# Performance work log

Hardware: AMD Instinct MI355X
Metric: run time of the kernel (lower is better)

Reference implementation:

```python
import jax, jax.numpy as jnp
import numpy as np
import math

# ---- architecture constants (match init_kwargs defaults of OfficialMamba3SISO) ----
D_MODEL = 1024
D_STATE = 128
EXPAND = 2
HEADDIM = 64
NGROUPS = 1
D_INNER = EXPAND * D_MODEL              # 2048
NHEADS = D_INNER // HEADDIM             # 32
ROPE_FRACTION = 0.5
SPLIT = int(D_STATE * ROPE_FRACTION)    # rotary span of the state dim
SPLIT -= SPLIT % 2                      # 64
NUM_ANGLES = SPLIT // 2                 # 32
A_FLOOR = 1e-4
EPS = 1e-5
DT_MIN, DT_MAX, DT_INIT_FLOOR = 1e-3, 1e-1, 1e-4
D_IN_PROJ = 2 * D_INNER + 2 * D_STATE * NGROUPS + 3 * NHEADS + NUM_ANGLES  # 4480


def _rmsnorm(x, w):
    xf = x.astype(jnp.float32)
    return xf * jax.lax.rsqrt(jnp.mean(xf * xf, axis=-1, keepdims=True) + EPS) * w


def _rope(v, theta):
    # rotate first SPLIT dims of the state axis by cumulative angles theta [..., NUM_ANGLES]
    v1 = v[..., :NUM_ANGLES]
    v2 = v[..., NUM_ANGLES:SPLIT]
    rest = v[..., SPLIT:]
    c, s = jnp.cos(theta), jnp.sin(theta)
    return jnp.concatenate([v1 * c - v2 * s, v1 * s + v2 * c, rest], axis=-1)


def setup_inputs() -> dict:
    key = jax.random.key(0)
    ks = jax.random.split(key, 6)
    b, l = 2, 1024
    u = jax.random.normal(ks[0], (b, l, D_MODEL), jnp.float32)
    W_in = jax.random.normal(ks[1], (D_IN_PROJ, D_MODEL), jnp.float32) * 0.02
    W_out = jax.random.normal(ks[2], (D_MODEL, D_INNER), jnp.float32) * 0.02
    # dt_bias init exactly as in the torch module
    _dt = jnp.exp(jax.random.uniform(ks[3], (NHEADS,), jnp.float32)
                  * (math.log(DT_MAX) - math.log(DT_MIN)) + math.log(DT_MIN))
    _dt = jnp.clip(_dt, DT_INIT_FLOOR, None)
    dt_bias = _dt + jnp.log(-jnp.expm1(-_dt))
    B_bias = jnp.ones((NHEADS, D_STATE), jnp.float32)   # mimo_rank=1 squeezed
    C_bias = jnp.ones((NHEADS, D_STATE), jnp.float32)
    B_norm_w = jnp.ones((D_STATE,), jnp.float32)
    C_norm_w = jnp.ones((D_STATE,), jnp.float32)
    D_param = jnp.ones((NHEADS,), jnp.float32)
    return {"u": u, "W_in": W_in, "W_out": W_out, "dt_bias": dt_bias,
            "B_bias": B_bias, "C_bias": C_bias, "B_norm_w": B_norm_w,
            "C_norm_w": C_norm_w, "D_param": D_param}


def reference(u, W_in, W_out, dt_bias, B_bias, C_bias, B_norm_w, C_norm_w, D_param):
    b, l, _ = u.shape
    proj = u @ W_in.T                                   # [b,l,4480]
    sizes = [D_INNER, D_INNER, D_STATE * NGROUPS, D_STATE * NGROUPS,
             NHEADS, NHEADS, NHEADS, NUM_ANGLES]
    splits = np.cumsum(sizes)[:-1]
    z, x, B, C, dd_dt, dd_A, trap, angles = jnp.split(proj, splits, axis=-1)
    z = z.reshape(b, l, NHEADS, HEADDIM)
    x = x.reshape(b, l, NHEADS, HEADDIM)
    B = B.reshape(b, l, NGROUPS, D_STATE)
    C = C.reshape(b, l, NGROUPS, D_STATE)

    a = -jax.nn.softplus(dd_A.astype(jnp.float32))
    a = jnp.minimum(a, -A_FLOOR)                        # [b,l,h]
    dt = jax.nn.softplus(dd_dt.astype(jnp.float32) + dt_bias)  # [b,l,h]
    adt = a * dt

    # RoPE-style angle cumsum: theta_t = sum_{s<=t} angle_s * dt_s (per head)
    theta = jnp.cumsum(angles[:, :, None, :].astype(jnp.float32) * dt[..., None], axis=1)  # [b,l,h,na]

    Bn = _rmsnorm(B, B_norm_w)                          # [b,l,g,n]
    Cn = _rmsnorm(C, C_norm_w)
    head_group = np.repeat(np.arange(NGROUPS), NHEADS // NGROUPS)
    Bh = Bn[:, :, head_group, :] + B_bias               # [b,l,h,n]
    Ch = Cn[:, :, head_group, :] + C_bias
    Bh = _rope(Bh, theta)
    Ch = _rope(Ch, theta)

    lam = jax.nn.sigmoid(trap.astype(jnp.float32))      # trapezoidal mixing, [b,l,h]
    g = jnp.exp(adt)                                    # decay, [b,l,h]

    xs = (jnp.moveaxis(x.astype(jnp.float32), 1, 0), jnp.moveaxis(Bh, 1, 0),
          jnp.moveaxis(Ch, 1, 0), jnp.moveaxis(dt, 1, 0),
          jnp.moveaxis(g, 1, 0), jnp.moveaxis(lam, 1, 0))
    h0 = jnp.zeros((b, NHEADS, HEADDIM, D_STATE), jnp.float32)
    bx0 = jnp.zeros_like(h0)

    def step(carry, inp):
        h, bx_prev = carry
        x_t, B_t, C_t, dt_t, g_t, lam_t = inp
        bx_t = x_t[..., :, None] * B_t[..., None, :]    # outer product [b,h,p,n]
        ge = g_t[..., None, None]
        dte = dt_t[..., None, None]
        le = lam_t[..., None, None]
        # generalized trapezoidal discretization (Mamba-3):
        # h_t = g_t h_{t-1} + dt_t * (lam_t B_t x_t + (1-lam_t) g_t B_{t-1} x_{t-1})
        h = ge * h + dte * (le * bx_t + (1.0 - le) * ge * bx_prev)
        y_t = jnp.einsum('bhpn,bhn->bhp', h, C_t)
        return (h, bx_t), y_t

    _, ys = jax.lax.scan(step, (h0, bx0), xs)
    y = jnp.moveaxis(ys, 0, 1) + D_param[:, None] * x   # skip term, [b,l,h,p]
    y = y * jax.nn.silu(z)                              # gated output (Z passed to kernel)
    y = y.reshape(b, l, D_INNER).astype(u.dtype)
    return y @ W_out.T
```

## Files before the change

kernel.cpp:

```cpp
#include <hip/hip_runtime.h>
#include <hip/hip_bf16.h>
#include <math.h>

#define BATCH 2
#define SEQ 1024
#define DMODEL 1024
#define DSTATE 128
#define HEADDIM 64
#define NHEADS 32
#define DINNER 2048
#define NUMANG 32
#define DPROJ 4480
#define CH 64
#define NCH 16
#define TAILSTART 4352
#define OFF_Z 0
#define OFF_X 2048
#define OFF_B 4096
#define OFF_C 4224
#define OFF_DT 4352
#define OFF_A 4384
#define OFF_TRAP 4416
#define OFF_ANG 4448

typedef __attribute__((ext_vector_type(8))) short bf16x8;
typedef __attribute__((ext_vector_type(4))) float f32x4;
typedef unsigned short u16;

__device__ __forceinline__ u16 f2bf(float f) {
  unsigned int u = __float_as_uint(f);
  u += 0x7FFFu + ((u >> 16) & 1u);
  return (u16)(u >> 16);
}
__device__ __forceinline__ float bf2f(u16 x) {
  return __uint_as_float(((unsigned int)x) << 16);
}

__global__ __launch_bounds__(256) void cvt_bf16(const float* __restrict__ in,
                                                u16* __restrict__ out, int n4) {
  int i = blockIdx.x * 256 + threadIdx.x;
  if (i >= n4) return;
  float4 v = ((const float4*)in)[i];
  ushort4 o;
  o.x = f2bf(v.x); o.y = f2bf(v.y); o.z = f2bf(v.z); o.w = f2bf(v.w);
  ((ushort4*)out)[i] = o;
}

__device__ __forceinline__ void gload_lds16(const void* g, void* l) {
  __builtin_amdgcn_global_load_lds(
      (const __attribute__((address_space(1))) unsigned int*)g,
      (__attribute__((address_space(3))) unsigned int*)l, 16, 0, 0);
}

__global__ __launch_bounds__(256) void gemm_proj64(const u16* __restrict__ A,
                                                   const u16* __restrict__ B,
                                                   u16* __restrict__ Cb,
                                                   float* __restrict__ tailF,
                                                   int M, int N, int K) {
  __shared__ u16 As[64 * 64];
  __shared__ u16 Bs[64 * 64];
  const int tid = threadIdx.x;
  const int lane = tid & 63, wave = tid >> 6;
  const int bm = blockIdx.y * 64, bn = blockIdx.x * 64;
  const int wm = (wave >> 1) * 32, wn = (wave & 1) * 32;
  const int srow = wave * 8 + (lane >> 3);
  const int scol = (((lane & 7) ^ ((lane >> 3) & 7)) * 8);
  const u16* Ab = A + (size_t)(bm + srow) * K + scol;
  const u16* Bb = B + (size_t)(bn + srow) * K + scol;
  u16* Asw = As + wave * 512;
  u16* Bsw = Bs + wave * 512;
  f32x4 acc[2][2];
#pragma unroll
  for (int i = 0; i < 2; ++i)
#pragma unroll
    for (int j = 0; j < 2; ++j) acc[i][j] = (f32x4){0.f, 0.f, 0.f, 0.f};
  const int fr = lane & 15, fq = lane >> 4, sw = fr & 7;

  for (int k0 = 0; k0 < K; k0 += 64) {
    __syncthreads();
#pragma unroll
    for (int it = 0; it < 2; ++it) {
      gload_lds16(Ab + (size_t)(it * 32) * K + k0, Asw + it * 2048);
      gload_lds16(Bb + (size_t)(it * 32) * K + k0, Bsw + it * 2048);
    }
    __syncthreads();
#pragma unroll
    for (int kh = 0; kh < 2; ++kh) {
      bf16x8 af[2], bfv[2];
#pragma unroll
      for (int i = 0; i < 2; ++i)
        af[i] = *(const bf16x8*)(As + (wm + i * 16 + fr) * 64 + (((kh * 4 + fq) ^ sw) * 8));
#pragma unroll
      for (int j = 0; j < 2; ++j)
        bfv[j] = *(const bf16x8*)(Bs + (wn + j * 16 + fr) * 64 + (((kh * 4 + fq) ^ sw) * 8));
#pragma unroll
      for (int i = 0; i < 2; ++i)
#pragma unroll
        for (int j = 0; j < 2; ++j)
          acc[i][j] = __builtin_amdgcn_mfma_f32_16x16x32_bf16(af[i], bfv[j], acc[i][j], 0, 0, 0);
    }
  }
  const int orow = bm + wm + fq * 4;
  const int ocol = bn + wn + fr;
  const bool tail = (bn >= TAILSTART);
#pragma unroll
  for (int i = 0; i < 2; ++i)
#pragma unroll
    for (int j = 0; j < 2; ++j)
#pragma unroll
      for (int r = 0; r < 4; ++r) {
        float v = acc[i][j][r];
        int row = orow + i * 16 + r, col = ocol + j * 16;
        Cb[(size_t)row * N + col] = f2bf(v);
        if (tail) tailF[(size_t)row * 128 + (col - TAILSTART)] = v;
      }
}

__global__ __launch_bounds__(256) void gemm_out64(const u16* __restrict__ A,
                                                  const u16* __restrict__ B,
                                                  float* __restrict__ C,
                                                  int M, int N, int K) {
  __shared__ u16 As[64 * 64];
  __shared__ u16 Bs[64 * 64];
  const int tid = threadIdx.x;
  const int lane = tid & 63, wave = tid >> 6;
  const int bm = blockIdx.y * 64, bn = blockIdx.x * 64;
  const int wm = (wave >> 1) * 32, wn = (wave & 1) * 32;
  const int srow = wave * 8 + (lane >> 3);
  const int scol = (((lane & 7) ^ ((lane >> 3) & 7)) * 8);
  const u16* Ab = A + (size_t)(bm + srow) * K + scol;
  const u16* Bb = B + (size_t)(bn + srow) * K + scol;
  u16* Asw = As + wave * 512;
  u16* Bsw = Bs + wave * 512;
  f32x4 acc[2][2];
#pragma unroll
  for (int i = 0; i < 2; ++i)
#pragma unroll
    for (int j = 0; j < 2; ++j) acc[i][j] = (f32x4){0.f, 0.f, 0.f, 0.f};
  const int fr = lane & 15, fq = lane >> 4, sw = fr & 7;

  for (int k0 = 0; k0 < K; k0 += 64) {
    __syncthreads();
#pragma unroll
    for (int it = 0; it < 2; ++it) {
      gload_lds16(Ab + (size_t)(it * 32) * K + k0, Asw + it * 2048);
      gload_lds16(Bb + (size_t)(it * 32) * K + k0, Bsw + it * 2048);
    }
    __syncthreads();
#pragma unroll
    for (int kh = 0; kh < 2; ++kh) {
      bf16x8 af[2], bfv[2];
#pragma unroll
      for (int i = 0; i < 2; ++i)
        af[i] = *(const bf16x8*)(As + (wm + i * 16 + fr) * 64 + (((kh * 4 + fq) ^ sw) * 8));
#pragma unroll
      for (int j = 0; j < 2; ++j)
        bfv[j] = *(const bf16x8*)(Bs + (wn + j * 16 + fr) * 64 + (((kh * 4 + fq) ^ sw) * 8));
#pragma unroll
      for (int i = 0; i < 2; ++i)
#pragma unroll
        for (int j = 0; j < 2; ++j)
          acc[i][j] = __builtin_amdgcn_mfma_f32_16x16x32_bf16(af[i], bfv[j], acc[i][j], 0, 0, 0);
    }
  }
  const int orow = bm + wm + fq * 4;
  const int ocol = bn + wn + fr;
#pragma unroll
  for (int i = 0; i < 2; ++i)
#pragma unroll
    for (int j = 0; j < 2; ++j)
#pragma unroll
      for (int r = 0; r < 4; ++r)
        C[(size_t)(orow + i * 16 + r) * N + ocol + j * 16] = acc[i][j][r];
}

__device__ __forceinline__ float softplusf(float x) {
  return fmaxf(x, 0.f) + log1pf(expf(-fabsf(x)));
}

__global__ __launch_bounds__(1024) void theta_kernel(const float* __restrict__ tailF,
                                                     const float* __restrict__ dt_bias,
                                                     float4* __restrict__ sc4,
                                                     float4* __restrict__ theta4) {
  __shared__ float4 part[16];
  __shared__ float4 part2[16];
  const int blk = blockIdx.x;
  const int bh = blk >> 3, kc = blk & 7;
  const int b = bh >> 5, h = bh & 31;
  const int l = threadIdx.x;
  const int lane = l & 63, w = l >> 6;
  const float* trow = tailF + (size_t)(b * SEQ + l) * 128;
  float ddt = trow[h];
  float dt = softplusf(ddt + dt_bias[h]);
  if (kc == 0) {
    float dda = trow[32 + h];
    float trp = trow[64 + h];
    float a = fminf(-softplusf(dda), -1e-4f);
    float adt = a * dt;
    float lam = 1.0f / (1.0f + expf(-trp));
    sc4[(size_t)bh * SEQ + l] = make_float4(dt, expf(adt), lam, adt);
  }
  float4 v = *(const float4*)(trow + 96 + kc * 4);
  v.x *= dt; v.y *= dt; v.z *= dt; v.w *= dt;
#pragma unroll
  for (int off = 1; off < 64; off <<= 1) {
    float tx = __shfl_up(v.x, off, 64);
    float ty = __shfl_up(v.y, off, 64);
    float tz = __shfl_up(v.z, off, 64);
    float tw = __shfl_up(v.w, off, 64);
    if (lane >= off) { v.x += tx; v.y += ty; v.z += tz; v.w += tw; }
  }
  if (lane == 63) part[w] = v;
  __syncthreads();
  if (l < 16) {
    float4 p = part[l];
#pragma unroll
    for (int off = 1; off < 16; off <<= 1) {
      float tx = __shfl_up(p.x, off, 16);
      float ty = __shfl_up(p.y, off, 16);
      float tz = __shfl_up(p.z, off, 16);
      float tw = __shfl_up(p.w, off, 16);
      if (l >= off) { p.x += tx; p.y += ty; p.z += tz; p.w += tw; }
    }
    part2[l] = p;
  }
  __syncthreads();
  if (w > 0) {
    float4 o = part2[w - 1];
    v.x += o.x; v.y += o.y; v.z += o.z; v.w += o.w;
  }
  theta4[((size_t)(b * SEQ + l) * NHEADS + h) * 8 + kc] = v;
}

__global__ __launch_bounds__(1024) void rope_kernel(const u16* __restrict__ proj16,
                                                    const float* __restrict__ theta,
                                                    const float* __restrict__ B_bias,
                                                    const float* __restrict__ C_bias,
                                                    const float* __restrict__ Bnw,
                                                    const float* __restrict__ Cnw,
                                                    u16* __restrict__ Bh,
                                                    u16* __restrict__ Ch) {
  const int bl = blockIdx.x;
  const int b = bl >> 10, l = bl & 1023;
  const int tid = threadIdx.x;
  __shared__ float sB[128], sC[128], red[4];
  __shared__ float cth[1024], sth[1024];
  float bv = 0.f, cv = 0.f;
  const size_t row = (size_t)bl * DPROJ;
  if (tid < 128) {
    bv = bf2f(proj16[row + OFF_B + tid]);
    cv = bf2f(proj16[row + OFF_C + tid]);
    float sb = bv * bv, sc = cv * cv;
    for (int m = 32; m; m >>= 1) { sb += __shfl_xor(sb, m); sc += __shfl_xor(sc, m); }
    const int wave = tid >> 6;
    if ((tid & 63) == 0) { red[wave * 2] = sb; red[wave * 2 + 1] = sc; }
  }
  {
    float th = theta[(size_t)bl * 1024 + tid];
    cth[tid] = cosf(th);
    sth[tid] = sinf(th);
  }
  __syncthreads();
  if (tid < 128) {
    float rb = rsqrtf((red[0] + red[2]) / 128.0f + 1e-5f);
    float rc = rsqrtf((red[1] + red[3]) / 128.0f + 1e-5f);
    sB[tid] = bv * rb * Bnw[tid];
    sC[tid] = cv * rc * Cnw[tid];
  }
  __syncthreads();
  const int h = tid >> 5;
  const int n0 = (tid & 31) * 4;
  float ob[4], oc[4];
  if (n0 < 32) {
#pragma unroll
    for (int j = 0; j < 4; ++j) {
      int n = n0 + j;
      float c = cth[h * 32 + n], s = sth[h * 32 + n];
      float b1 = sB[n] + B_bias[h * 128 + n];
      float b2 = sB[n + 32] + B_bias[h * 128 + n + 32];
      float c1 = sC[n] + C_bias[h * 128 + n];
      float c2 = sC[n + 32] + C_bias[h * 128 + n + 32];
      ob[j] = b1 * c - b2 * s;
      oc[j] = c1 * c - c2 * s;
    }
  } else if (n0 < 64) {
#pragma unroll
    for (int j = 0; j < 4; ++j) {
      int n = n0 + j, k = n - 32;
      float c = cth[h * 32 + k], s = sth[h * 32 + k];
      float b1 = sB[k] + B_bias[h * 128 + k];
      float b2 = sB[k + 32] + B_bias[h * 128 + k + 32];
      float c1 = sC[k] + C_bias[h * 128 + k];
      float c2 = sC[k + 32] + C_bias[h * 128 + k + 32];
      ob[j] = b1 * s + b2 * c;
      oc[j] = c1 * s + c2 * c;
    }
  } else {
#pragma unroll
    for (int j = 0; j < 4; ++j) {
      int n = n0 + j;
      ob[j] = sB[n] + B_bias[h * 128 + n];
      oc[j] = sC[n] + C_bias[h * 128 + n];
    }
  }
  size_t o = (((size_t)(b * NHEADS + h)) * SEQ + l) * DSTATE + n0;
  ushort4 vb = {f2bf(ob[0]), f2bf(ob[1]), f2bf(ob[2]), f2bf(ob[3])};
  ushort4 vc = {f2bf(oc[0]), f2bf(oc[1]), f2bf(oc[2]), f2bf(oc[3])};
  *(ushort4*)&Bh[o] = vb;
  *(ushort4*)&Ch[o] = vc;
}

#define SWB 136
#define SWS 72

__global__ __launch_bounds__(256) void chunk_kernel(
    const u16* __restrict__ proj16,
    const float4* __restrict__ sc4,
    const u16* __restrict__ Bh16,
    const u16* __restrict__ Ch16,
    u16* __restrict__ Ybuf,
    float* __restrict__ dHT,
    float* __restrict__ Gv_g,
    float2* __restrict__ de_g) {
  __shared__ u16 sCb[64 * SWB];
  __shared__ u16 sBb[64 * SWB];
  __shared__ u16 sBt[128 * SWS];
  __shared__ u16 sXt[64 * SWS];
  __shared__ u16 sSw[64 * SWS];
  __shared__ float sA[64], sW[64], sDL[64], sCV[64];

  const int blk = blockIdx.x;
  const int bh = blk >> 4, ch = blk & 15;
  const int b = bh >> 5, h = bh & 31;
  const int t0 = ch * CH;
  const int tid = threadIdx.x;
  const int lane = tid & 63, wave = tid >> 6;

  {
    const int row = tid >> 5;
    const int c4 = tid & 31;
#pragma unroll
    for (int pass = 0; pass < 8; ++pass) {
      int ll = pass * 8 + row;
      int l = t0 + ll;
      ushort4 cv = *(const ushort4*)&Ch16[((size_t)bh * SEQ + l) * DSTATE + c4 * 4];
      ushort4 bv = *(const ushort4*)&Bh16[((size_t)bh * SEQ + l) * DSTATE + c4 * 4];
      *(ushort4*)&sCb[ll * SWB + c4 * 4] = cv;
      *(ushort4*)&sBb[ll * SWB + c4 * 4] = bv;
      sBt[(c4 * 4 + 0) * SWS + ll] = bv.x;
      sBt[(c4 * 4 + 1) * SWS + ll] = bv.y;
      sBt[(c4 * 4 + 2) * SWS + ll] = bv.z;
      sBt[(c4 * 4 + 3) * SWS + ll] = bv.w;
    }
    const int xr = tid >> 2, xc = tid & 3;
    const u16* xrow = &proj16[(size_t)(b * SEQ + t0 + xr) * DPROJ + OFF_X + h * 64];
#pragma unroll
    for (int j = 0; j < 4; ++j) {
      ushort4 xv = *(const ushort4*)(xrow + xc * 16 + j * 4);
      int p = xc * 16 + j * 4;
      sXt[(p + 0) * SWS + xr] = xv.x;
      sXt[(p + 1) * SWS + xr] = xv.y;
      sXt[(p + 2) * SWS + xr] = xv.z;
      sXt[(p + 3) * SWS + xr] = xv.w;
    }
  }
  if (tid < 64) {
    float4 s = sc4[(size_t)bh * SEQ + t0 + tid];
    float dt = s.x, lam = s.z, adt = s.w;
    float A = adt;
#pragma unroll
    for (int off = 1; off < 64; off <<= 1) {
      float t = __shfl_up(A, off, 64);
      if (tid >= off) A += t;
    }
    float dtn = __shfl_down(dt, 1, 64);
    float lamn = __shfl_down(lam, 1, 64);
    float dl = dt * lam;
    float w = dl + dtn * (1.0f - lamn);
    if (tid == 63) w = 0.0f;
    float A63 = __shfl(A, 63, 64);
    float cv = (tid < 63) ? expf(A63 - A) * w : dl;
    sA[tid] = A; sW[tid] = w; sCV[tid] = cv; sDL[tid] = dl;
    Gv_g[((size_t)bh * NCH + ch) * 64 + tid] = expf(A);
    if (tid == 0) de_g[(size_t)bh * NCH + ch] = make_float2(expf(A63), dt * (1.0f - lam));
  }
  __syncthreads();

  const int fr = lane & 15, fq = lane >> 4;

  {
    f32x4 acc[4];
#pragma unroll
    for (int j = 0; j < 4; ++j) acc[j] = (f32x4){0.f, 0.f, 0.f, 0.f};
#pragma unroll
    for (int kc = 0; kc < 4; ++kc) {
      bf16x8 af = *(const bf16x8*)&sBb[(wave * 16 + fr) * SWB + kc * 32 + fq * 8];
#pragma unroll
      for (int j = 0; j < 4; ++j) {
        bf16x8 bf = *(const bf16x8*)&sCb[(j * 16 + fr) * SWB + kc * 32 + fq * 8];
        acc[j] = __builtin_amdgcn_mfma_f32_16x16x32_bf16(af, bf, acc[j], 0, 0, 0);
      }
    }
    const int sbase = wave * 16 + fq * 4;
#pragma unroll
    for (int j = 0; j < 4; ++j) {
      int t = j * 16 + fr;
      float At = sA[t], dlt = sDL[t];
#pragma unroll
      for (int r = 0; r < 4; ++r) {
        int ss = sbase + r;
        float f = (ss < t) ? expf(At - sA[ss]) * sW[ss] : ((ss == t) ? dlt : 0.0f);
        sSw[t * SWS + ss] = f2bf(acc[j][r] * f);
      }
    }
  }
  __syncthreads();

  {
    f32x4 acc[4];
#pragma unroll
    for (int j = 0; j < 4; ++j) acc[j] = (f32x4){0.f, 0.f, 0.f, 0.f};
#pragma unroll
    for (int kc = 0; kc < 2; ++kc) {
      bf16x8 af = *(const bf16x8*)&sSw[(wave * 16 + fr) * SWS + kc * 32 + fq * 8];
#pragma unroll
      for (int j = 0; j < 4; ++j) {
        bf16x8 bf = *(const bf16x8*)&sXt[(j * 16 + fr) * SWS + kc * 32 + fq * 8];
        acc[j] = __builtin_amdgcn_mfma_f32_16x16x32_bf16(af, bf, acc[j], 0, 0, 0);
      }
    }
    const int tr = t0 + wave * 16 + fq * 4;
#pragma unroll
    for (int j = 0; j < 4; ++j) {
      int p = j * 16 + fr;
#pragma unroll
      for (int r = 0; r < 4; ++r)
        Ybuf[(size_t)(b * SEQ + tr + r) * DINNER + h * 64 + p] = f2bf(acc[j][r]);
    }
  }
  __syncthreads();

  {
    const int p = tid >> 2;
    const int s0 = (tid & 3) * 16;
#pragma unroll
    for (int k = 0; k < 16; ++k) {
      int s = s0 + k;
      sXt[p * SWS + s] = f2bf(bf2f(sXt[p * SWS + s]) * sCV[s]);
    }
  }
  __syncthreads();

  {
#pragma unroll
    for (int mi = 0; mi < 2; ++mi) {
      f32x4 acc[4];
#pragma unroll
      for (int j = 0; j < 4; ++j) acc[j] = (f32x4){0.f, 0.f, 0.f, 0.f};
      const int nrow = wave * 32 + mi * 16;
#pragma unroll
      for (int kc = 0; kc < 2; ++kc) {
        bf16x8 af = *(const bf16x8*)&sBt[(nrow + fr) * SWS + kc * 32 + fq * 8];
#pragma unroll
        for (int j = 0; j < 4; ++j) {
          bf16x8 bf = *(const bf16x8*)&sXt[(j * 16 + fr) * SWS + kc * 32 + fq * 8];
          acc[j] = __builtin_amdgcn_mfma_f32_16x16x32_bf16(af, bf, acc[j], 0, 0, 0);
        }
      }
      const int nr = nrow + fq * 4;
#pragma unroll
      for (int j = 0; j < 4; ++j) {
        int p = j * 16 + fr;
#pragma unroll
        for (int r = 0; r < 4; ++r)
          dHT[(((size_t)bh * NCH + ch) * 128 + nr + r) * 64 + p] = acc[j][r];
      }
    }
  }
}

__global__ __launch_bounds__(512) void carry_kernel(
    const u16* __restrict__ proj16,
    const u16* __restrict__ Bh16,
    const float* __restrict__ dHT,
    const float2* __restrict__ de_g,
    float* __restrict__ Heff) {
  const int bh = blockIdx.x;
  const int b = bh >> 5, h = bh & 31;
  const int tid = threadIdx.x;
  const int n = tid >> 2;
  const int p0 = (tid & 3) * 16;
  float hreg[16] = {};
  for (int c = 0; c < NCH; ++c) {
    float2 de = de_g[bh * NCH + c];
    float heff[16];
    if (c == 0) {
#pragma unroll
      for (int j = 0; j < 16; ++j) heff[j] = 0.0f;
    } else {
      int lprev = c * CH - 1;
      float Bp = bf2f(Bh16[((size_t)bh * SEQ + lprev) * DSTATE + n]);
      const u16* xp = &proj16[(size_t)(b * SEQ + lprev) * DPROJ + OFF_X + h * 64 + p0];
      float eB = de.y * Bp;
#pragma unroll
      for (int j4 = 0; j4 < 4; ++j4) {
        ushort4 xv = *(const ushort4*)(xp + j4 * 4);
        heff[j4 * 4 + 0] = hreg[j4 * 4 + 0] + eB * bf2f(xv.x);
        heff[j4 * 4 + 1] = hreg[j4 * 4 + 1] + eB * bf2f(xv.y);
        heff[j4 * 4 + 2] = hreg[j4 * 4 + 2] + eB * bf2f(xv.z);
        heff[j4 * 4 + 3] = hreg[j4 * 4 + 3] + eB * bf2f(xv.w);
      }
    }
    size_t base = (((size_t)bh * NCH + c) * 128 + n) * 64 + p0;
#pragma unroll
    for (int j4 = 0; j4 < 4; ++j4)
      *(float4*)&Heff[base + j4 * 4] = *(const float4*)&heff[j4 * 4];
#pragma unroll
    for (int j4 = 0; j4 < 4; ++j4) {
      float4 dh = *(const float4*)&dHT[base + j4 * 4];
      hreg[j4 * 4 + 0] = de.x * heff[j4 * 4 + 0] + dh.x;
      hreg[j4 * 4 + 1] = de.x * heff[j4 * 4 + 1] + dh.y;
      hreg[j4 * 4 + 2] = de.x * heff[j4 * 4 + 2] + dh.z;
      hreg[j4 * 4 + 3] = de.x * heff[j4 * 4 + 3] + dh.w;
    }
  }
}

__global__ __launch_bounds__(256) void inter_kernel(
    const u16* __restrict__ proj16,
    const u16* __restrict__ Ch16,
    const float* __restrict__ Heff,
    const float* __restrict__ Gv_g,
    const float* __restrict__ Dp,
    u16* __restrict__ Ybuf) {
  __shared__ float sC[64][132];
  __shared__ float sH[128][68];
  __shared__ float sGv[64];
  const int blk = blockIdx.x;
  const int bh = blk >> 4, ch = blk & 15;
  const int b = bh >> 5, h = bh & 31;
  const int t0 = ch * CH;
  const int tid = threadIdx.x;
  {
    const int row = tid >> 5, c4 = tid & 31;
#pragma unroll
    for (int pass = 0; pass < 8; ++pass) {
      int l = t0 + pass * 8 + row;
      ushort4 cv = *(const ushort4*)&Ch16[((size_t)bh * SEQ + l) * DSTATE + c4 * 4];
      float4 cf = {bf2f(cv.x), bf2f(cv.y), bf2f(cv.z), bf2f(cv.w)};
      *(float4*)&sC[pass * 8 + row][c4 * 4] = cf;
    }
    const int hr = tid >> 4, hc = tid & 15;
#pragma unroll
    for (int pass = 0; pass < 8; ++pass) {
      int n = pass * 16 + hr;
      float4 hv = *(const float4*)&Heff[(((size_t)bh * NCH + ch) * 128 + n) * 64 + hc * 4];
      *(float4*)&sH[n][hc * 4] = hv;
    }
    if (tid < 64) sGv[tid] = Gv_g[((size_t)bh * NCH + ch) * 64 + tid];
  }
  __syncthreads();
  const int ty = tid >> 4, tx = tid & 15;
  float acc[4][4] = {};
  for (int n = 0; n < 128; n += 4) {
    float4 cv[4], hv[4];
#pragma unroll
    for (int i = 0; i < 4; ++i) cv[i] = *(const float4*)&sC[ty * 4 + i][n];
#pragma unroll
    for (int k = 0; k < 4; ++k) hv[k] = *(const float4*)&sH[n + k][tx * 4];
#pragma unroll
    for (int k = 0; k < 4; ++k) {
      const float* hp = (const float*)&hv[k];
#pragma unroll
      for (int i = 0; i < 4; ++i) {
        float cva = ((const float*)&cv[i])[k];
#pragma unroll
        for (int j = 0; j < 4; ++j)
          acc[i][j] = fmaf(cva, hp[j], acc[i][j]);
      }
    }
  }
  const float Dv = Dp[h];
#pragma unroll
  for (int i = 0; i < 4; ++i) {
    int l = t0 + ty * 4 + i;
    float gt = sGv[ty * 4 + i];
    size_t rowp = (size_t)(b * SEQ + l) * DPROJ;
    ushort4 xv = *(const ushort4*)&proj16[rowp + OFF_X + h * 64 + tx * 4];
    ushort4 zv = *(const ushort4*)&proj16[rowp + OFF_Z + h * 64 + tx * 4];
    size_t yo = (size_t)(b * SEQ + l) * DINNER + h * 64 + tx * 4;
    ushort4 y1 = *(const ushort4*)&Ybuf[yo];
    float x[4] = {bf2f(xv.x), bf2f(xv.y), bf2f(xv.z), bf2f(xv.w)};
    float z[4] = {bf2f(zv.x), bf2f(zv.y), bf2f(zv.z), bf2f(zv.w)};
    float y[4] = {bf2f(y1.x), bf2f(y1.y), bf2f(y1.z), bf2f(y1.w)};
    ushort4 o;
    u16* op = (u16*)&o;
#pragma unroll
    for (int j = 0; j < 4; ++j) {
      float yy = y[j] + gt * acc[i][j] + Dv * x[j];
      float sg = 1.0f / (1.0f + expf(-z[j]));
      op[j] = f2bf(yy * z[j] * sg);
    }
    *(ushort4*)&Ybuf[yo] = o;
  }
}

extern "C" void kernel_launch(void* const* d_in, const int* in_sizes, int n_in,
                              void* d_out, int out_size, void* d_ws, size_t ws_size,
                              hipStream_t stream) {
  const float* u       = (const float*)d_in[0];
  const float* W_in    = (const float*)d_in[1];
  const float* W_out   = (const float*)d_in[2];
  const float* dt_bias = (const float*)d_in[3];
  const float* B_bias  = (const float*)d_in[4];
  const float* C_bias  = (const float*)d_in[5];
  const float* Bnw     = (const float*)d_in[6];
  const float* Cnw     = (const float*)d_in[7];
  const float* Dp      = (const float*)d_in[8];
  float* out = (float*)d_out;

  char* ws = (char*)d_ws;
  u16*    proj16 = (u16*)(ws);
  float*  tailF  = (float*)(ws + 18350080);
  float4* sc4    = (float4*)(ws + 19398656);
  float*  theta  = (float*)(ws + 20447232);
  u16*    Bh16   = (u16*)(ws + 28835840);
  u16*    Ch16   = (u16*)(ws + 45613056);
  u16*    Ybuf   = (u16*)(ws + 62390272);
  float*  dHT    = (float*)(ws + 70778880);
  float*  Heff   = (float*)(ws + 104333312);
  float*  Gv     = (float*)(ws + 137887744);
  float2* deg    = (float2*)(ws + 138149888);
  u16*    ub16   = (u16*)(ws + 138158080);
  u16*    Wi16   = (u16*)(ws + 142352384);
  u16*    Wo16   = (u16*)(ws + 151527424);

  cvt_bf16<<<2048, 256, 0, stream>>>(u, ub16, 524288);
  cvt_bf16<<<4480, 256, 0, stream>>>(W_in, Wi16, 1146880);
  gemm_proj64<<<dim3(DPROJ / 64, (BATCH * SEQ) / 64), 256, 0, stream>>>(
      ub16, Wi16, proj16, tailF, BATCH * SEQ, DPROJ, DMODEL);
  theta_kernel<<<BATCH * NHEADS * 8, 1024, 0, stream>>>(tailF, dt_bias, sc4, (float4*)theta);
  rope_kernel<<<BATCH * SEQ, 1024, 0, stream>>>(proj16, theta, B_bias, C_bias, Bnw, Cnw, Bh16, Ch16);
  chunk_kernel<<<BATCH * NHEADS * NCH, 256, 0, stream>>>(
      proj16, sc4, Bh16, Ch16, Ybuf, dHT, Gv, deg);
  carry_kernel<<<BATCH * NHEADS, 512, 0, stream>>>(proj16, Bh16, dHT, deg, Heff);
  inter_kernel<<<BATCH * NHEADS * NCH, 256, 0, stream>>>(
      proj16, Ch16, Heff, Gv, Dp, Ybuf);
  cvt_bf16<<<2048, 256, 0, stream>>>(W_out, Wo16, 524288);
  gemm_out64<<<dim3(DMODEL / 64, (BATCH * SEQ) / 64), 256, 0, stream>>>(
      Ybuf, Wo16, out, BATCH * SEQ, DMODEL, DINNER);
}
```

Measured before the change: 270.8 us.

## Store chunk states as bf16 p-major, use MFMA in inter kernel, merge conversions

Chunk state deltas (dHT) and effective carried states (Heff) are now stored as bf16 in a [p][n] layout instead of fp32 [n][p], halving their memory traffic. The inter-chunk C·H product moves from a scalar fp32 FMA loop to bf16 MFMA, and the carry kernel is split into 4 blocks per head to get more parallelism. The three fp32-to-bf16 conversion launches are merged into one. The trade-off is lower precision in the carried state and strided 2-byte scalar stores in the epilogue.

```diff
diff --git a/kernel.cpp b/kernel.cpp
--- a/kernel.cpp
+++ b/kernel.cpp
@@ -36,14 +36,28 @@
   return __uint_as_float(((unsigned int)x) << 16);
 }
 
-__global__ __launch_bounds__(256) void cvt_bf16(const float* __restrict__ in,
-                                                u16* __restrict__ out, int n4) {
+#define N4_U 524288
+#define N4_WI 1146880
+#define N4_WO 524288
+
+__global__ __launch_bounds__(256) void cvt_all(const float* __restrict__ u,
+                                               const float* __restrict__ Wi,
+                                               const float* __restrict__ Wo,
+                                               u16* __restrict__ ub16,
+                                               u16* __restrict__ Wi16,
+                                               u16* __restrict__ Wo16) {
   int i = blockIdx.x * 256 + threadIdx.x;
-  if (i >= n4) return;
-  float4 v = ((const float4*)in)[i];
+  const float4* src;
+  ushort4* dst;
+  int idx;
+  if (i < N4_U) { src = (const float4*)u; dst = (ushort4*)ub16; idx = i; }
+  else if (i < N4_U + N4_WI) { src = (const float4*)Wi; dst = (ushort4*)Wi16; idx = i - N4_U; }
+  else if (i < N4_U + N4_WI + N4_WO) { src = (const float4*)Wo; dst = (ushort4*)Wo16; idx = i - N4_U - N4_WI; }
+  else return;
+  float4 v = src[idx];
   ushort4 o;
   o.x = f2bf(v.x); o.y = f2bf(v.y); o.z = f2bf(v.z); o.w = f2bf(v.w);
-  ((ushort4*)out)[i] = o;
+  dst[idx] = o;
 }
 
 __device__ __forceinline__ void gload_lds16(const void* g, void* l) {
@@ -319,7 +333,7 @@
     const u16* __restrict__ Bh16,
     const u16* __restrict__ Ch16,
     u16* __restrict__ Ybuf,
-    float* __restrict__ dHT,
+    u16* __restrict__ dHT16,
     float* __restrict__ Gv_g,
     float2* __restrict__ de_g) {
   __shared__ u16 sCb[64 * SWB];
@@ -452,44 +466,41 @@
   __syncthreads();
 
   {
-#pragma unroll
-    for (int mi = 0; mi < 2; ++mi) {
-      f32x4 acc[4];
-#pragma unroll
-      for (int j = 0; j < 4; ++j) acc[j] = (f32x4){0.f, 0.f, 0.f, 0.f};
-      const int nrow = wave * 32 + mi * 16;
-#pragma unroll
-      for (int kc = 0; kc < 2; ++kc) {
-        bf16x8 af = *(const bf16x8*)&sBt[(nrow + fr) * SWS + kc * 32 + fq * 8];
-#pragma unroll
-        for (int j = 0; j < 4; ++j) {
-          bf16x8 bf = *(const bf16x8*)&sXt[(j * 16 + fr) * SWS + kc * 32 + fq * 8];
-          acc[j] = __builtin_amdgcn_mfma_f32_16x16x32_bf16(af, bf, acc[j], 0, 0, 0);
-        }
+    f32x4 acc[8];
+#pragma unroll
+    for (int j = 0; j < 8; ++j) acc[j] = (f32x4){0.f, 0.f, 0.f, 0.f};
+#pragma unroll
+    for (int kc = 0; kc < 2; ++kc) {
+      bf16x8 af = *(const bf16x8*)&sXt[(wave * 16 + fr) * SWS + kc * 32 + fq * 8];
+#pragma unroll
+      for (int j = 0; j < 8; ++j) {
+        bf16x8 bf = *(const bf16x8*)&sBt[(j * 16 + fr) * SWS + kc * 32 + fq * 8];
+        acc[j] = __builtin_amdgcn_mfma_f32_16x16x32_bf16(af, bf, acc[j], 0, 0, 0);
       }
-      const int nr = nrow + fq * 4;
-#pragma unroll
-      for (int j = 0; j < 4; ++j) {
-        int p = j * 16 + fr;
-#pragma unroll
-        for (int r = 0; r < 4; ++r)
-          dHT[(((size_t)bh * NCH + ch) * 128 + nr + r) * 64 + p] = acc[j][r];
-      }
-    }
-  }
-}
-
-__global__ __launch_bounds__(512) void carry_kernel(
+    }
+    const int pr = wave * 16 + fq * 4;
+#pragma unroll
+    for (int j = 0; j < 8; ++j) {
+      int n = j * 16 + fr;
+#pragma unroll
+      for (int r = 0; r < 4; ++r)
+        dHT16[(((size_t)bh * NCH + ch) * 64 + pr + r) * 128 + n] = f2bf(acc[j][r]);
+    }
+  }
+}
+
+__global__ __launch_bounds__(128) void carry_kernel(
     const u16* __restrict__ proj16,
     const u16* __restrict__ Bh16,
-    const float* __restrict__ dHT,
+    const u16* __restrict__ dHT16,
     const float2* __restrict__ de_g,
-    float* __restrict__ Heff) {
-  const int bh = blockIdx.x;
+    u16* __restrict__ Heff16) {
+  const int blk = blockIdx.x;
+  const int bh = blk >> 2, pg = blk & 3;
   const int b = bh >> 5, h = bh & 31;
   const int tid = threadIdx.x;
-  const int n = tid >> 2;
-  const int p0 = (tid & 3) * 16;
+  const int p = pg * 16 + (tid >> 3);
+  const int n0 = (tid & 7) * 16;
   float hreg[16] = {};
   for (int c = 0; c < NCH; ++c) {
     float2 de = de_g[bh * NCH + c];
@@ -499,29 +510,32 @@
       for (int j = 0; j < 16; ++j) heff[j] = 0.0f;
     } else {
       int lprev = c * CH - 1;
-      float Bp = bf2f(Bh16[((size_t)bh * SEQ + lprev) * DSTATE + n]);
-      const u16* xp = &proj16[(size_t)(b * SEQ + lprev) * DPROJ + OFF_X + h * 64 + p0];
-      float eB = de.y * Bp;
+      float xp = bf2f(proj16[(size_t)(b * SEQ + lprev) * DPROJ + OFF_X + h * 64 + p]);
+      float eBx = de.y * xp;
+      const u16* Bp = &Bh16[((size_t)bh * SEQ + lprev) * DSTATE + n0];
 #pragma unroll
       for (int j4 = 0; j4 < 4; ++j4) {
-        ushort4 xv = *(const ushort4*)(xp + j4 * 4);
-        heff[j4 * 4 + 0] = hreg[j4 * 4 + 0] + eB * bf2f(xv.x);
-        heff[j4 * 4 + 1] = hreg[j4 * 4 + 1] + eB * bf2f(xv.y);
-        heff[j4 * 4 + 2] = hreg[j4 * 4 + 2] + eB * bf2f(xv.z);
-        heff[j4 * 4 + 3] = hreg[j4 * 4 + 3] + eB * bf2f(xv.w);
+        ushort4 bv = *(const ushort4*)(Bp + j4 * 4);
+        heff[j4 * 4 + 0] = hreg[j4 * 4 + 0] + eBx * bf2f(bv.x);
+        heff[j4 * 4 + 1] = hreg[j4 * 4 + 1] + eBx * bf2f(bv.y);
+        heff[j4 * 4 + 2] = hreg[j4 * 4 + 2] + eBx * bf2f(bv.z);
+        heff[j4 * 4 + 3] = hreg[j4 * 4 + 3] + eBx * bf2f(bv.w);
       }
     }
-    size_t base = (((size_t)bh * NCH + c) * 128 + n) * 64 + p0;
-#pragma unroll
-    for (int j4 = 0; j4 < 4; ++j4)
-      *(float4*)&Heff[base + j4 * 4] = *(const float4*)&heff[j4 * 4];
+    size_t base = (((size_t)bh * NCH + c) * 64 + p) * 128 + n0;
 #pragma unroll
     for (int j4 = 0; j4 < 4; ++j4) {
-      float4 dh = *(const float4*)&dHT[base + j4 * 4];
-      hreg[j4 * 4 + 0] = de.x * heff[j4 * 4 + 0] + dh.x;
-      hreg[j4 * 4 + 1] = de.x * heff[j4 * 4 + 1] + dh.y;
-      hreg[j4 * 4 + 2] = de.x * heff[j4 * 4 + 2] + dh.z;
-      hreg[j4 * 4 + 3] = de.x * heff[j4 * 4 + 3] + dh.w;
+      ushort4 o = {f2bf(heff[j4 * 4 + 0]), f2bf(heff[j4 * 4 + 1]),
+                   f2bf(heff[j4 * 4 + 2]), f2bf(heff[j4 * 4 + 3])};
+      *(ushort4*)&Heff16[base + j4 * 4] = o;
+    }
+#pragma unroll
+    for (int j4 = 0; j4 < 4; ++j4) {
+      ushort4 dh = *(const ushort4*)&dHT16[base + j4 * 4];
+      hreg[j4 * 4 + 0] = de.x * heff[j4 * 4 + 0] + bf2f(dh.x);
+      hreg[j4 * 4 + 1] = de.x * heff[j4 * 4 + 1] + bf2f(dh.y);
+      hreg[j4 * 4 + 2] = de.x * heff[j4 * 4 + 2] + bf2f(dh.z);
+      hreg[j4 * 4 + 3] = de.x * heff[j4 * 4 + 3] + bf2f(dh.w);
     }
   }
 }
@@ -529,79 +543,64 @@
 __global__ __launch_bounds__(256) void inter_kernel(
     const u16* __restrict__ proj16,
     const u16* __restrict__ Ch16,
-    const float* __restrict__ Heff,
+    const u16* __restrict__ Heff16,
     const float* __restrict__ Gv_g,
     const float* __restrict__ Dp,
     u16* __restrict__ Ybuf) {
-  __shared__ float sC[64][132];
-  __shared__ float sH[128][68];
+  __shared__ u16 sCt[64 * SWB];
+  __shared__ u16 sHe[64 * SWB];
   __shared__ float sGv[64];
   const int blk = blockIdx.x;
   const int bh = blk >> 4, ch = blk & 15;
   const int b = bh >> 5, h = bh & 31;
   const int t0 = ch * CH;
   const int tid = threadIdx.x;
+  const int lane = tid & 63, wave = tid >> 6;
   {
-    const int row = tid >> 5, c4 = tid & 31;
-#pragma unroll
-    for (int pass = 0; pass < 8; ++pass) {
-      int l = t0 + pass * 8 + row;
-      ushort4 cv = *(const ushort4*)&Ch16[((size_t)bh * SEQ + l) * DSTATE + c4 * 4];
-      float4 cf = {bf2f(cv.x), bf2f(cv.y), bf2f(cv.z), bf2f(cv.w)};
-      *(float4*)&sC[pass * 8 + row][c4 * 4] = cf;
-    }
-    const int hr = tid >> 4, hc = tid & 15;
-#pragma unroll
-    for (int pass = 0; pass < 8; ++pass) {
-      int n = pass * 16 + hr;
-      float4 hv = *(const float4*)&Heff[(((size_t)bh * NCH + ch) * 128 + n) * 64 + hc * 4];
-      *(float4*)&sH[n][hc * 4] = hv;
+    const int row = tid >> 2, seg = tid & 3;
+    const u16* csrc = &Ch16[((size_t)bh * SEQ + t0 + row) * DSTATE + seg * 32];
+    const u16* hsrc = &Heff16[(((size_t)bh * NCH + ch) * 64 + row) * 128 + seg * 32];
+#pragma unroll
+    for (int q = 0; q < 4; ++q) {
+      *(ushort4*)&sCt[row * SWB + seg * 32 + q * 8]     = *(const ushort4*)(csrc + q * 8);
+      *(ushort4*)&sCt[row * SWB + seg * 32 + q * 8 + 4] = *(const ushort4*)(csrc + q * 8 + 4);
+      *(ushort4*)&sHe[row * SWB + seg * 32 + q * 8]     = *(const ushort4*)(hsrc + q * 8);
+      *(ushort4*)&sHe[row * SWB + seg * 32 + q * 8 + 4] = *(const ushort4*)(hsrc + q * 8 + 4);
     }
     if (tid < 64) sGv[tid] = Gv_g[((size_t)bh * NCH + ch) * 64 + tid];
   }
   __syncthreads();
-  const int ty = tid >> 4, tx = tid & 15;
-  float acc[4][4] = {};
-  for (int n = 0; n < 128; n += 4) {
-    float4 cv[4], hv[4];
-#pragma unroll
-    for (int i = 0; i < 4; ++i) cv[i] = *(const float4*)&sC[ty * 4 + i][n];
-#pragma unroll
-    for (int k = 0; k < 4; ++k) hv[k] = *(const float4*)&sH[n + k][tx * 4];
-#pragma unroll
-    for (int k = 0; k < 4; ++k) {
-      const float* hp = (const float*)&hv[k];
-#pragma unroll
-      for (int i = 0; i < 4; ++i) {
-        float cva = ((const float*)&cv[i])[k];
-#pragma unroll
-        for (int j = 0; j < 4; ++j)
-          acc[i][j] = fmaf(cva, hp[j], acc[i][j]);
-      }
+  const int fr = lane & 15, fq = lane >> 4;
+  f32x4 acc[4];
+#pragma unroll
+  for (int j = 0; j < 4; ++j) acc[j] = (f32x4){0.f, 0.f, 0.f, 0.f};
+#pragma unroll
+  for (int kc = 0; kc < 4; ++kc) {
+    bf16x8 af = *(const bf16x8*)&sCt[(wave * 16 + fr) * SWB + kc * 32 + fq * 8];
+#pragma unroll
+    for (int j = 0; j < 4; ++j) {
+      bf16x8 bf = *(const bf16x8*)&sHe[(j * 16 + fr) * SWB + kc * 32 + fq * 8];
+      acc[j] = __builtin_amdgcn_mfma_f32_16x16x32_bf16(af, bf, acc[j], 0, 0, 0);
     }
   }
   const float Dv = Dp[h];
 #pragma unroll
-  for (int i = 0; i < 4; ++i) {
-    int l = t0 + ty * 4 + i;
-    float gt = sGv[ty * 4 + i];
+  for (int r = 0; r < 4; ++r) {
+    int tl = wave * 16 + fq * 4 + r;
+    int l = t0 + tl;
+    float gt = sGv[tl];
     size_t rowp = (size_t)(b * SEQ + l) * DPROJ;
-    ushort4 xv = *(const ushort4*)&proj16[rowp + OFF_X + h * 64 + tx * 4];
-    ushort4 zv = *(const ushort4*)&proj16[rowp + OFF_Z + h * 64 + tx * 4];
-    size_t yo = (size_t)(b * SEQ + l) * DINNER + h * 64 + tx * 4;
-    ushort4 y1 = *(const ushort4*)&Ybuf[yo];
-    float x[4] = {bf2f(xv.x), bf2f(xv.y), bf2f(xv.z), bf2f(xv.w)};
-    float z[4] = {bf2f(zv.x), bf2f(zv.y), bf2f(zv.z), bf2f(zv.w)};
-    float y[4] = {bf2f(y1.x), bf2f(y1.y), bf2f(y1.z), bf2f(y1.w)};
-    ushort4 o;
-    u16* op = (u16*)&o;
-#pragma unroll
-    for (int j = 0; j < 4; ++j) {
-      float yy = y[j] + gt * acc[i][j] + Dv * x[j];
-      float sg = 1.0f / (1.0f + expf(-z[j]));
-      op[j] = f2bf(yy * z[j] * sg);
-    }
-    *(ushort4*)&Ybuf[yo] = o;
+    size_t yrow = (size_t)(b * SEQ + l) * DINNER + h * 64;
+#pragma unroll
+    for (int j = 0; j < 4; ++j) {
+      int p = j * 16 + fr;
+      float x = bf2f(proj16[rowp + OFF_X + h * 64 + p]);
+      float z = bf2f(proj16[rowp + OFF_Z + h * 64 + p]);
+      float y1 = bf2f(Ybuf[yrow + p]);
+      float yy = y1 + gt * acc[j][r] + Dv * x;
+      float sg = 1.0f / (1.0f + expf(-z));
+      Ybuf[yrow + p] = f2bf(yy * z * sg);
+    }
   }
 }
 
@@ -627,26 +626,25 @@
   u16*    Bh16   = (u16*)(ws + 28835840);
   u16*    Ch16   = (u16*)(ws + 45613056);
   u16*    Ybuf   = (u16*)(ws + 62390272);
-  float*  dHT    = (float*)(ws + 70778880);
-  float*  Heff   = (float*)(ws + 104333312);
-  float*  Gv     = (float*)(ws + 137887744);
-  float2* deg    = (float2*)(ws + 138149888);
-  u16*    ub16   = (u16*)(ws + 138158080);
-  u16*    Wi16   = (u16*)(ws + 142352384);
-  u16*    Wo16   = (u16*)(ws + 151527424);
-
-  cvt_bf16<<<2048, 256, 0, stream>>>(u, ub16, 524288);
-  cvt_bf16<<<4480, 256, 0, stream>>>(W_in, Wi16, 1146880);
+  u16*    dHT16  = (u16*)(ws + 70778880);
+  u16*    Heff16 = (u16*)(ws + 87556096);
+  float*  Gv     = (float*)(ws + 104333312);
+  float2* deg    = (float2*)(ws + 104595456);
+  u16*    ub16   = (u16*)(ws + 104603648);
+  u16*    Wi16   = (u16*)(ws + 108797952);
+  u16*    Wo16   = (u16*)(ws + 117972992);
+
+  cvt_all<<<(N4_U + N4_WI + N4_WO + 255) / 256, 256, 0, stream>>>(
+      u, W_in, W_out, ub16, Wi16, Wo16);
   gemm_proj64<<<dim3(DPROJ / 64, (BATCH * SEQ) / 64), 256, 0, stream>>>(
       ub16, Wi16, proj16, tailF, BATCH * SEQ, DPROJ, DMODEL);
   theta_kernel<<<BATCH * NHEADS * 8, 1024, 0, stream>>>(tailF, dt_bias, sc4, (float4*)theta);
   rope_kernel<<<BATCH * SEQ, 1024, 0, stream>>>(proj16, theta, B_bias, C_bias, Bnw, Cnw, Bh16, Ch16);
   chunk_kernel<<<BATCH * NHEADS * NCH, 256, 0, stream>>>(
-      proj16, sc4, Bh16, Ch16, Ybuf, dHT, Gv, deg);
-  carry_kernel<<<BATCH * NHEADS, 512, 0, stream>>>(proj16, Bh16, dHT, deg, Heff);
+      proj16, sc4, Bh16, Ch16, Ybuf, dHT16, Gv, deg);
+  carry_kernel<<<BATCH * NHEADS * 4, 128, 0, stream>>>(proj16, Bh16, dHT16, deg, Heff16);
   inter_kernel<<<BATCH * NHEADS * NCH, 256, 0, stream>>>(
-      proj16, Ch16, Heff, Gv, Dp, Ybuf);
-  cvt_bf16<<<2048, 256, 0, stream>>>(W_out, Wo16, 524288);
+      proj16, Ch16, Heff16, Gv, Dp, Ybuf);
   gemm_out64<<<dim3(DMODEL / 64, (BATCH * SEQ) / 64), 256, 0, stream>>>(
       Ybuf, Wo16, out, BATCH * SEQ, DMODEL, DINNER);
 }
```

Result: faster. 231.0 us (median of 2 runs) (-14.7%).
